# Performance work log

Measured on AMD Instinct MI355X. Metric: run time of the kernel, lower is better.

Reference implementation:

```python
import jax, jax.numpy as jnp
import numpy as np

N_Q = 8        # qubits
DENC = 3       # encoding entangling layers
DVAR = 3       # variational entangling layers
SEQ = 64
BATCH = 256
D_FEAT = N_Q * (DENC + 2)   # 40, per-token feature dim
D_W = N_Q * (DVAR + 2)      # 40, per-position weight dim


def _rx(t):
    c = jnp.cos(t / 2).astype(jnp.complex64)
    s = (-1j * jnp.sin(t / 2)).astype(jnp.complex64)
    return jnp.stack([jnp.stack([c, s]), jnp.stack([s, c])])


def _ry(t):
    c = jnp.cos(t / 2)
    s = jnp.sin(t / 2)
    return jnp.stack([jnp.stack([c, -s]), jnp.stack([s, c])]).astype(jnp.complex64)


def _apply1(state, U, wire):
    # state: (2,)*N_Q complex; apply 2x2 gate on `wire`
    s = jnp.tensordot(U, state, axes=([1], [wire]))
    return jnp.moveaxis(s, 0, wire)


def _cnot(state, c, t):
    s0 = jnp.take(state, 0, axis=c)
    s1 = jnpp_flip = jnp.take(state, 1, axis=c)
    t2 = t - 1 if t > c else t
    s1 = jnp.flip(s1, axis=t2)  # X on target when control=1
    return jnp.stack([s0, s1], axis=c)


def _circuit(x, w, sign):
    # x: [D_FEAT] encoding angles, w: [D_W] variational angles
    state = jnp.zeros((2,) * N_Q, jnp.complex64).at[(0,) * N_Q].set(1.0)
    idx = 0
    for j in range(N_Q):
        state = _apply1(state, _rx(x[idx]), j)
        state = _apply1(state, _ry(x[idx + 1]), j)
        idx += 2
    for _ in range(DENC):
        for j in range(N_Q):
            state = _cnot(state, j, (j + 1) % N_Q)
        for j in range(N_Q):
            state = _apply1(state, _ry(x[idx]), j)
            idx += 1
    idx = 0
    for j in range(N_Q):
        state = _apply1(state, _rx(w[idx]), j)
        state = _apply1(state, _ry(w[idx + 1]), j)
        idx += 2
    for _ in range(DVAR):
        for j in range(N_Q):
            state = _cnot(state, j, (j + 1) % N_Q)
        for j in range(N_Q):
            state = _apply1(state, _ry(w[idx]), j)
            idx += 1
    probs = (jnp.abs(state) ** 2).astype(jnp.float32)
    return jnp.sum(probs * sign)


# observable sign tables
_Z0 = jnp.array([1.0, -1.0], jnp.float32).reshape((2,) + (1,) * (N_Q - 1))
_ZALL = jnp.array([1.0, -1.0], jnp.float32)
for _ in range(N_Q - 1):
    _ZALL = _ZALL[..., None] * jnp.array([1.0, -1.0], jnp.float32)


def _batched(sign):
    f = lambda xx, ww: _circuit(xx, ww, sign)
    f = jax.vmap(f, in_axes=(0, 0))      # over seq positions (per-position weights)
    return jax.vmap(f, in_axes=(0, None))  # over batch


_qk = _batched(_Z0)
_v = _batched(_ZALL)  # random_op fixed deterministically to Z x Z x ... x Z


def setup_inputs() -> dict:
    key = jax.random.key(0)
    k1, k2, k3, k4 = jax.random.split(key, 4)
    scale = np.float32(np.pi / 4)
    x = jax.random.normal(k1, (BATCH, SEQ, D_FEAT), jnp.float32)
    pQ = scale * (2 * jax.random.normal(k2, (SEQ, D_W), jnp.float32) - 1)
    pK = scale * (2 * jax.random.normal(k3, (SEQ, D_W), jnp.float32) - 1)
    pV = scale * (2 * jax.random.normal(k4, (SEQ, D_W), jnp.float32) - 1)
    return {"x": x, "params_Q": pQ, "params_K": pK, "params_V": pV}


def reference(x, params_Q, params_K, params_V):
    # Per-token quantum circuit sims -> scalar Q, K, V expectations
    Q = _qk(x, params_Q)   # [B, S]
    K = _qk(x, params_K)   # [B, S]
    V = _v(x, params_V)    # [B, S]  (original returns d identical copies of this)
    # Gaussian-kernel attention: alpha[b,i,m] = exp(-(Q_i - K_m)^2)
    alpha = jnp.exp(-(Q[:, :, None] - K[:, None, :]) ** 2)   # [B, S, S]
    w = alpha / jnp.sum(alpha, axis=-1, keepdims=True)
    att = jnp.einsum('bim,bm->bi', w, V)                     # [B, S]
    return x + att[:, :, None]  # broadcast over d (V copies are identical)
```

## Files before the change

### kernel.cpp

```cpp
#include <hip/hip_runtime.h>

#define SEQd 64
#define BATCHd 256
#define DF 40

typedef float f2 __attribute__((ext_vector_type(2)));
typedef __fp16 h2v __attribute__((ext_vector_type(2)));


__device__ __forceinline__ f2 mkf2(float a, float b) { f2 r; r.x = a; r.y = b; return r; }

template<int LM>
__device__ __forceinline__ float xch1(float v) {
  if constexpr (LM == 0) {
    return v;
  } else if constexpr (LM == 1 || LM == 2 || LM == 3 || LM == 7 || LM == 15) {
    constexpr int ctrl = (LM == 1) ? 0xB1 : (LM == 2) ? 0x4E : (LM == 3) ? 0x1B
                       : (LM == 7) ? 0x141 : 0x140;
    return __int_as_float(__builtin_amdgcn_mov_dpp(__float_as_int(v), ctrl, 0xF, 0xF, true));
  } else if constexpr (LM == 4)  { return xch1<7>(xch1<3>(v));
  } else if constexpr (LM == 5)  { return xch1<7>(xch1<2>(v));
  } else if constexpr (LM == 6)  { return xch1<7>(xch1<1>(v));
  } else if constexpr (LM == 8)  { return xch1<15>(xch1<7>(v));
  } else if constexpr (LM == 12) { return xch1<15>(xch1<3>(v));
  } else if constexpr (LM == 13) { return xch1<15>(xch1<2>(v));
  } else if constexpr (LM == 14) { return xch1<15>(xch1<1>(v));
  } else {
    return __int_as_float(__builtin_amdgcn_ds_swizzle(__float_as_int(v), (LM << 10) | 0x1F));
  }
}

template<int LM>
__device__ __forceinline__ f2 xch2(f2 v) {
  if constexpr (LM == 0) return v;
  f2 r; r.x = xch1<LM>(v.x); r.y = xch1<LM>(v.y); return r;
}

__device__ __forceinline__ f2 pkmul(f2 a, f2 b) {
  f2 d;
  asm("v_pk_mul_f32 %0, %1, %2" : "=v"(d) : "v"(a), "v"(b));
  return d;
}
template<bool NEGB, bool SWAPA>
__device__ __forceinline__ f2 pkfma(f2 a, f2 b, f2 c) {
  f2 d;
  if constexpr (!NEGB && !SWAPA)
    asm("v_pk_fma_f32 %0, %1, %2, %3" : "=v"(d) : "v"(a), "v"(b), "v"(c));
  else if constexpr (NEGB && !SWAPA)
    asm("v_pk_fma_f32 %0, %1, %2, %3 neg_lo:[0,1,0] neg_hi:[0,1,0]"
        : "=v"(d) : "v"(a), "v"(b), "v"(c));
  else if constexpr (!NEGB && SWAPA)
    asm("v_pk_fma_f32 %0, %1, %2, %3 op_sel:[1,0,0] op_sel_hi:[0,1,1]"
        : "=v"(d) : "v"(a), "v"(b), "v"(c));
  else
    asm("v_pk_fma_f32 %0, %1, %2, %3 op_sel:[1,0,0] op_sel_hi:[0,1,1] neg_lo:[0,1,0] neg_hi:[0,1,0]"
        : "=v"(d) : "v"(a), "v"(b), "v"(c));
  return d;
}

__device__ __forceinline__ f2 cmul(f2 a, f2 b) {
  f2 r; r.x = a.x * b.x - a.y * b.y; r.y = a.x * b.y + a.y * b.x; return r;
}
__device__ __forceinline__ f2 uget(float4 f, bool bit) {
  f2 r; r.x = bit ? f.z : f.x; r.y = bit ? -f.w : f.y; return r;
}

template<int M, int SM, int J>
__device__ __forceinline__ void ry_rec(f2* rr, f2* ii, f2 CC, f2 TV) {
  if constexpr (J < 8) {
    constexpr int LM = M >> 4, RM = M & 15;
    constexpr int RJ = RM >> 1;
    constexpr bool R0 = (RM & 1) != 0;
    constexpr int JP = J ^ RJ;
    if constexpr (JP >= J) {
      constexpr int SRj = (SM & 15) >> 1;
      constexpr bool PJ = (__builtin_popcount(J & SRj) & 1) != 0;
      if constexpr (JP == J) {
        const f2 br = xch2<LM>(rr[J]);
        const f2 bi = xch2<LM>(ii[J]);
        rr[J] = pkfma<PJ, R0>(br, TV, pkmul(rr[J], CC));
        ii[J] = pkfma<PJ, R0>(bi, TV, pkmul(ii[J], CC));
      } else {
        constexpr bool PJP = (__builtin_popcount(JP & SRj) & 1) != 0;
        const f2 br0 = xch2<LM>(rr[JP]);
        const f2 bi0 = xch2<LM>(ii[JP]);
        const f2 br1 = xch2<LM>(rr[J]);
        const f2 bi1 = xch2<LM>(ii[J]);
        rr[J]  = pkfma<PJ,  R0>(br0, TV, pkmul(rr[J],  CC));
        ii[J]  = pkfma<PJ,  R0>(bi0, TV, pkmul(ii[J],  CC));
        rr[JP] = pkfma<PJP, R0>(br1, TV, pkmul(rr[JP], CC));
        ii[JP] = pkfma<PJP, R0>(bi1, TV, pkmul(ii[JP], CC));
      }
    }
    ry_rec<M, SM, J + 1>(rr, ii, CC, TV);
  }
}

template<int M, int SM>
__device__ __forceinline__ void ry16s(f2* rr, f2* ii, f2 cs, int lam) {
  constexpr int SL = SM >> 4;
  constexpr bool S0v = (SM & 1) != 0;
  float t0;
  if constexpr (SL != 0) t0 = (__popc(lam & SL) & 1) ? cs.y : -cs.y;
  else                   t0 = -cs.y;
  const f2 CC = mkf2(cs.x, cs.x);
  const f2 TV = mkf2(t0, S0v ? -t0 : t0);
  ry_rec<M, SM, 0>(rr, ii, CC, TV);
}

template<int M, int SM, int J>
__device__ __forceinline__ void su2_rec(f2* rr, f2* ii, f2 QX, f2 QW, f2 SC, f2 SB) {
  if constexpr (J < 8) {
    constexpr int LM = M >> 4, RM = M & 15;
    constexpr int RJ = RM >> 1;
    constexpr bool R0 = (RM & 1) != 0;
    constexpr int JP = J ^ RJ;
    if constexpr (JP >= J) {
      constexpr int SRj = (SM & 15) >> 1;
      constexpr bool PJ = (__builtin_popcount(J & SRj) & 1) != 0;
      if constexpr (JP == J) {
        const f2 br = xch2<LM>(rr[J]);
        const f2 bi = xch2<LM>(ii[J]);
        f2 t = pkmul(rr[J], QX);
        t = pkfma<!PJ, R0>(br, SC, t);
        t = pkfma<!PJ, false>(ii[J], SB, t);
        t = pkfma<false, R0>(bi, QW, t);
        f2 u = pkmul(ii[J], QX);
        u = pkfma<!PJ, R0>(bi, SC, u);
        u = pkfma<PJ, false>(rr[J], SB, u);
        u = pkfma<true, R0>(br, QW, u);
        rr[J] = t; ii[J] = u;
      } else {
        constexpr bool PJP = (__builtin_popcount(JP & SRj) & 1) != 0;
        const f2 br0 = xch2<LM>(rr[JP]);
        const f2 bi0 = xch2<LM>(ii[JP]);
        const f2 br1 = xch2<LM>(rr[J]);
        const f2 bi1 = xch2<LM>(ii[J]);
        f2 t0v = pkmul(rr[J], QX);
        t0v = pkfma<!PJ, R0>(br0, SC, t0v);
        t0v = pkfma<!PJ, false>(ii[J], SB, t0v);
        t0v = pkfma<false, R0>(bi0, QW, t0v);
        f2 u0v = pkmul(ii[J], QX);
        u0v = pkfma<!PJ, R0>(bi0, SC, u0v);
        u0v = pkfma<PJ, false>(rr[J], SB, u0v);
        u0v = pkfma<true, R0>(br0, QW, u0v);
        f2 t1v = pkmul(rr[JP], QX);
        t1v = pkfma<!PJP, R0>(br1, SC, t1v);
        t1v = pkfma<!PJP, false>(ii[JP], SB, t1v);
        t1v = pkfma<false, R0>(bi1, QW, t1v);
        f2 u1v = pkmul(ii[JP], QX);
        u1v = pkfma<!PJP, R0>(bi1, SC, u1v);
        u1v = pkfma<PJP, false>(rr[JP], SB, u1v);
        u1v = pkfma<true, R0>(br1, QW, u1v);
        rr[J] = t0v; ii[J] = u0v; rr[JP] = t1v; ii[JP] = u1v;
      }
    }
    su2_rec<M, SM, J + 1>(rr, ii, QX, QW, SC, SB);
  }
}

template<int M, int SM>
__device__ __forceinline__ void su2g(f2* rr, f2* ii, float4 q, int lam) {
  constexpr int SL = SM >> 4;
  constexpr bool S0v = (SM & 1) != 0;
  float sb, sc;
  if constexpr (SL != 0) {
    const bool p = (__popc(lam & SL) & 1) != 0;
    sb = p ? -q.y : q.y; sc = p ? -q.z : q.z;
  } else { sb = q.y; sc = q.z; }
  const f2 QX = mkf2(q.x, q.x), QW = mkf2(q.w, q.w);
  const f2 SCv = mkf2(sc, S0v ? -sc : sc);
  const f2 SBv = mkf2(sb, S0v ? -sb : sb);
  su2_rec<M, SM, 0>(rr, ii, QX, QW, SCv, SBv);
}

__device__ __forceinline__ void layers16s(f2* rr, f2* ii, const f2* L, int lam) {
  ry16s<0xC0,0x7F>(rr, ii, L[0],  lam);
  ry16s<0x60,0xC0>(rr, ii, L[1],  lam);
  ry16s<0x30,0xE0>(rr, ii, L[2],  lam);
  ry16s<0x18,0xF0>(rr, ii, L[3],  lam);
  ry16s<0x0C,0xF8>(rr, ii, L[4],  lam);
  ry16s<0x06,0xFC>(rr, ii, L[5],  lam);
  ry16s<0x03,0xFE>(rr, ii, L[6],  lam);
  ry16s<0xC1,0xFF>(rr, ii, L[7],  lam);
  ry16s<0xA0,0xD5>(rr, ii, L[8],  lam);
  ry16s<0x50,0xBF>(rr, ii, L[9],  lam);
  ry16s<0x28,0x5F>(rr, ii, L[10], lam);
  ry16s<0x14,0xAF>(rr, ii, L[11], lam);
  ry16s<0x0A,0x57>(rr, ii, L[12], lam);
  ry16s<0x05,0xAB>(rr, ii, L[13], lam);
  ry16s<0xC2,0x55>(rr, ii, L[14], lam);
  ry16s<0x61,0xAA>(rr, ii, L[15], lam);
  ry16s<0xF0,0x4C>(rr, ii, L[16], lam);
  ry16s<0x78,0x6A>(rr, ii, L[17], lam);
  ry16s<0x3C,0x35>(rr, ii, L[18], lam);
  ry16s<0x1E,0x9A>(rr, ii, L[19], lam);
  ry16s<0x0F,0xCD>(rr, ii, L[20], lam);
  ry16s<0xC7,0x66>(rr, ii, L[21], lam);
  ry16s<0xA3,0x33>(rr, ii, L[22], lam);
  ry16s<0x91,0x99>(rr, ii, L[23], lam);
}

__device__ __forceinline__ void initial16s(f2* rr, f2* ii, const float4* F, int lam) {
  su2g<0x80,0x80>(rr, ii, F[0], lam);
  su2g<0x40,0x40>(rr, ii, F[1], lam);
  su2g<0x20,0x20>(rr, ii, F[2], lam);
  su2g<0x10,0x10>(rr, ii, F[3], lam);
  su2g<0x08,0x08>(rr, ii, F[4], lam);
  su2g<0x04,0x04>(rr, ii, F[5], lam);
  su2g<0x02,0x02>(rr, ii, F[6], lam);
  su2g<0x01,0x01>(rr, ii, F[7], lam);
}

__device__ __forceinline__ void pinit16s(f2* rr, f2* ii, const float4* F, int lam) {
  f2 c = mkf2(1.f, 0.f);
#pragma unroll
  for (int i = 0; i < 4; ++i)
    c = cmul(c, uget(F[3 - i], ((lam >> i) & 1) != 0));
  f2 w67[4], w45[4];
#pragma unroll
  for (int j = 0; j < 4; ++j) {
    w67[j] = cmul(uget(F[6], (j & 2) != 0), uget(F[7], (j & 1) != 0));
    w45[j] = cmul(uget(F[4], (j & 2) != 0), uget(F[5], (j & 1) != 0));
  }
#pragma unroll
  for (int k = 0; k < 16; ++k) {
    const f2 u = w67[k & 3], w = w45[(k >> 2) & 3];
    f2 t = cmul(u, w);
    const f2 a = cmul(c, t);
    rr[k >> 1][k & 1] = a.x;
    ii[k >> 1][k & 1] = a.y;
  }
}

__device__ __forceinline__ uint32_t packh(float a, float b) {
  h2v h = __builtin_amdgcn_cvt_pkrtz(a, b);
  return __builtin_bit_cast(uint32_t, h);
}
__device__ __forceinline__ f2 unpackh(uint32_t u) {
  h2v h = __builtin_bit_cast(h2v, u);
  f2 r; r.x = (float)h[0]; r.y = (float)h[1]; return r;
}

__device__ __forceinline__ void snap_write16s(const f2* rr, const f2* ii,
                                              uint32_t* sn, int lam) {
  int tgt = 0;
  if (lam & 1) tgt ^= 0x33;
  if (lam & 2) tgt ^= 0x66;
  if (lam & 4) tgt ^= 0xCC;
  if (lam & 8) tgt ^= 0x19;
#pragma unroll
  for (int k = 0; k < 16; ++k) {
    const int rck = ((k & 1) ? 0x2B : 0) ^ ((k & 2) ? 0x56 : 0)
                  ^ ((k & 4) ? 0xAC : 0) ^ ((k & 8) ? 0xD9 : 0);
    sn[tgt ^ rck] = packh(rr[k >> 1][k & 1], ii[k >> 1][k & 1]);
  }
}

__device__ __forceinline__ void snap_read16s(f2* rr, f2* ii, const uint32_t* sn, int lam) {
  const uint4* p = (const uint4*)(sn + lam * 16);
#pragma unroll
  for (int t = 0; t < 4; ++t) {
    const uint4 w = p[t];
    const f2 a0 = unpackh(w.x), a1 = unpackh(w.y), a2 = unpackh(w.z), a3 = unpackh(w.w);
    rr[2 * t]     = mkf2(a0.x, a1.x);  ii[2 * t]     = mkf2(a0.y, a1.y);
    rr[2 * t + 1] = mkf2(a2.x, a3.x);  ii[2 * t + 1] = mkf2(a2.y, a3.y);
  }
}

template<int SM>
__device__ __forceinline__ float expect16s(const f2* rr, const f2* ii, int lam) {
  constexpr int SL = SM >> 4, SR4 = SM & 15;
  constexpr int SRj = SR4 >> 1;
  constexpr bool S0v = (SR4 & 1) != 0;
  float d = 0.f;
#pragma unroll
  for (int j = 0; j < 8; ++j) {
    const f2 pp = pkfma<false, false>(ii[j], ii[j], pkmul(rr[j], rr[j]));
    float contrib;
    if constexpr (S0v) contrib = pp.x - pp.y;
    else               contrib = pp.x + pp.y;
    const bool pj = (__builtin_popcount(j & SRj) & 1) != 0;
    d += pj ? -contrib : contrib;
  }
  float v;
  if constexpr (SL != 0) v = (__popc(lam & SL) & 1) ? -d : d;
  else                   v = d;
  v += xch1<1>(v); v += xch1<2>(v); v += xch1<4>(v); v += xch1<8>(v);
  return v;
}

__global__ __launch_bounds__(256) void prep_var(
    const float* __restrict__ pQ, const float* __restrict__ pK,
    const float* __restrict__ pV, float* __restrict__ vtab)
{
  const int t = blockIdx.x * 256 + threadIdx.x;
  if (t >= SEQd * 3 * 32) return;
  const int slot = t & 31;
  const int sh = t >> 5;
  const int h = sh % 3, sp = sh / 3;
  const float* w = ((h == 0) ? pQ : (h == 1) ? pK : pV) + sp * DF;
  float* o = vtab + sh * 80;
  if (slot < 8) {
    float cx, sx, cy, sy;
    __sincosf(w[2 * slot]     * 0.5f, &sx, &cx);
    __sincosf(w[2 * slot + 1] * 0.5f, &sy, &cy);
    ((float4*)o)[slot] = make_float4(cy * cx, sy * sx, sy * cx, cy * sx);
  } else {
    float sn, cn;
    __sincosf(w[16 + (slot - 8)] * 0.5f, &sn, &cn);
    ((float2*)(o + 32))[slot - 8] = make_float2(cn, sn);
  }
}

__global__ __launch_bounds__(256, 3) void qsal_mono(
    const float* __restrict__ x, const float* __restrict__ vtab,
    float* __restrict__ Qo, float* __restrict__ Ko, float* __restrict__ Vo)
{
  __shared__ __align__(16) float etab[16][84];
  __shared__ __align__(16) uint32_t snap[16][264];
  __shared__ __align__(16) float vtabs[240];
  const int tid = threadIdx.x;
  const int wid = tid >> 6, lane = tid & 63;
  const int lam = lane & 15;
  const int cig = (wid << 2) | (lane >> 4);
  const int s = blockIdx.x & 63;
  const int bbase = (blockIdx.x >> 6) << 4;

  for (int t = tid; t < 640; t += 256) {
    const int cc = t / 40, idx = t - cc * 40;
    const float ang = x[((size_t)(bbase + cc) * 64 + s) * 40 + idx];
    float sn, cn; __sincosf(ang * 0.5f, &sn, &cn);
    if (idx < 16) {
      const int wire = idx >> 1, isy = idx & 1;
      etab[cc][wire * 4 + isy * 2 + 0] = cn;
      etab[cc][wire * 4 + isy * 2 + 1] = sn;
    } else {
      etab[cc][32 + (idx - 16) * 2 + 0] = cn;
      etab[cc][32 + (idx - 16) * 2 + 1] = sn;
    }
  }
  if (tid < 60) ((float4*)vtabs)[tid] = ((const float4*)(vtab + s * 240))[tid];
  __syncthreads();
  if (tid < 128) {
    const int cc = tid >> 3, wire = tid & 7;
    float4* qt = (float4*)etab[cc];
    const float4 f = qt[wire];
    qt[wire] = make_float4(f.z * f.x, f.w * f.y, f.w * f.x, f.z * f.y);
  }
  __syncthreads();

  f2 rr[8], ii[8];
#pragma unroll 1
  for (int ph = 0; ph < 4; ++ph) {
    const f2* L;
    if (ph == 0) {
      pinit16s(rr, ii, (const float4*)etab[cig], lam);
      L = (const f2*)(etab[cig] + 32);
    } else {
      snap_read16s(rr, ii, snap[cig], lam);
      const float* th = vtabs + (ph - 1) * 80;
      initial16s(rr, ii, (const float4*)th, lam);
      L = (const f2*)(th + 32);
    }
    layers16s(rr, ii, L, lam);
    if (ph == 0) {
      snap_write16s(rr, ii, snap[cig], lam);
    } else {
      const float e = (ph == 3) ? expect16s<0x88>(rr, ii, lam)
                                : expect16s<0x4C>(rr, ii, lam);
      if (lam == 0) {
        float* op = (ph == 1) ? Qo : (ph == 2) ? Ko : Vo;
        op[(bbase + cig) * 64 + s] = e;
      }
    }
  }
}

__global__ __launch_bounds__(256) void qsal_attn(
    const float* __restrict__ x,
    const float* __restrict__ Qv,
    const float* __restrict__ Kv,
    const float* __restrict__ Vv,
    float* __restrict__ out)
{
  const int tid  = threadIdx.x;
  const int wid  = tid >> 6;
  const int lane = tid & 63;
  const int bi   = blockIdx.x * 4 + wid;
  const int b    = bi >> 6;

  const float q = Qv[bi];
  const float k = Kv[b * 64 + lane];
  const float v = Vv[b * 64 + lane];
  const float d = q - k;
  float e  = __expf(-d * d);
  float ev = e * v;
#pragma unroll
  for (int m = 1; m < 64; m <<= 1) {
    e  += __shfl_xor(e,  m, 64);
    ev += __shfl_xor(ev, m, 64);
  }
  const float att = ev / e;

  const size_t row = (size_t)bi * DF;
  if (lane < DF) out[row + lane] = x[row + lane] + att;
}

extern "C" void kernel_launch(void* const* d_in, const int* in_sizes, int n_in,
                              void* d_out, int out_size, void* d_ws, size_t ws_size,
                              hipStream_t stream) {
  const float* x  = (const float*)d_in[0];
  const float* pQ = (const float*)d_in[1];
  const float* pK = (const float*)d_in[2];
  const float* pV = (const float*)d_in[3];
  float* out = (float*)d_out;

  const int NC = BATCHd * SEQd;
  float* Qv   = (float*)d_ws;
  float* Kv   = Qv + NC;
  float* Vv   = Kv + NC;
  float* vtab = Vv + NC;

  prep_var<<<dim3(24), dim3(256), 0, stream>>>(pQ, pK, pV, vtab);
  qsal_mono<<<dim3(1024), dim3(256), 0, stream>>>(x, vtab, Qv, Kv, Vv);
  qsal_attn<<<dim3(NC / 4), dim3(256), 0, stream>>>(x, Qv, Kv, Vv, out);
}
```

Measured before the change: 82.94 us.

## Split monolithic circuit kernel into encoding and variational kernels via global snapshots

The single qsal_mono kernel is replaced, when the workspace is large enough, by two kernels. The first runs the encoding circuit per token and writes the packed state snapshot to global memory. The second launches three times as many blocks, each applying one of the Q/K/V variational circuits and computing its expectation. This aims to raise parallelism and occupancy (launch bounds 6) in the variational stage. In exchange it adds a 16 MB global round trip of snapshot data, plus an extra launch.

```diff
diff --git a/kernel.cpp b/kernel.cpp
--- a/kernel.cpp
+++ b/kernel.cpp
@@ -313,6 +313,83 @@
   }
 }
 
+__global__ __launch_bounds__(256, 3) void qsal_enc16(
+    const float* __restrict__ x, uint32_t* __restrict__ snapg)
+{
+  __shared__ __align__(16) float etab[16][84];
+  __shared__ __align__(16) uint32_t snap[16][264];
+  const int tid = threadIdx.x;
+  const int wid = tid >> 6, lane = tid & 63;
+  const int lam = lane & 15;
+  const int cig = (wid << 2) | (lane >> 4);
+  const int s = blockIdx.x & 63;
+  const int bbase = (blockIdx.x >> 6) << 4;
+
+  for (int t = tid; t < 640; t += 256) {
+    const int cc = t / 40, idx = t - cc * 40;
+    const float ang = x[((size_t)(bbase + cc) * 64 + s) * 40 + idx];
+    float sn, cn; __sincosf(ang * 0.5f, &sn, &cn);
+    if (idx < 16) {
+      const int wire = idx >> 1, isy = idx & 1;
+      etab[cc][wire * 4 + isy * 2 + 0] = cn;
+      etab[cc][wire * 4 + isy * 2 + 1] = sn;
+    } else {
+      etab[cc][32 + (idx - 16) * 2 + 0] = cn;
+      etab[cc][32 + (idx - 16) * 2 + 1] = sn;
+    }
+  }
+  __syncthreads();
+  if (tid < 128) {
+    const int cc = tid >> 3, wire = tid & 7;
+    float4* qt = (float4*)etab[cc];
+    const float4 f = qt[wire];
+    qt[wire] = make_float4(f.z * f.x, f.w * f.y, f.w * f.x, f.z * f.y);
+  }
+  __syncthreads();
+
+  f2 rr[8], ii[8];
+  pinit16s(rr, ii, (const float4*)etab[cig], lam);
+  layers16s(rr, ii, (const f2*)(etab[cig] + 32), lam);
+  snap_write16s(rr, ii, snap[cig], lam);
+
+  const int gw = (bbase + cig) * 64 + s;
+  uint4* gb = (uint4*)(snapg + (size_t)gw * 256);
+  const uint4* ls = (const uint4*)&snap[cig][lam * 16];
+#pragma unroll
+  for (int t = 0; t < 4; ++t) gb[lam * 4 + t] = ls[t];
+}
+
+__global__ __launch_bounds__(256, 6) void qsal_var16(
+    const uint32_t* __restrict__ snapg, const float* __restrict__ vtab,
+    float* __restrict__ Qo, float* __restrict__ Ko, float* __restrict__ Vo)
+{
+  __shared__ __align__(16) float ltab[84];
+  const int tid = threadIdx.x;
+  const int wid = tid >> 6, lane = tid & 63;
+  const int lam = lane & 15;
+  const int cig = (wid << 2) | (lane >> 4);
+  const int vb = blockIdx.x;
+  const int s = vb / 48;
+  const int j = vb - s * 48;
+  const int grp = j / 3, h = j - grp * 3;
+
+  if (tid < 20)
+    ((float4*)ltab)[tid] = ((const float4*)(vtab + (s * 3 + h) * 80))[tid];
+  __syncthreads();
+
+  const int gw = (grp * 16 + cig) * 64 + s;
+  f2 rr[8], ii[8];
+  snap_read16s(rr, ii, snapg + (size_t)gw * 256, lam);
+  initial16s(rr, ii, (const float4*)ltab, lam);
+  layers16s(rr, ii, (const f2*)(ltab + 32), lam);
+  const float e = (h == 2) ? expect16s<0x88>(rr, ii, lam)
+                           : expect16s<0x4C>(rr, ii, lam);
+  if (lam == 0) {
+    float* op = (h == 0) ? Qo : (h == 1) ? Ko : Vo;
+    op[gw] = e;
+  }
+}
+
 __global__ __launch_bounds__(256, 3) void qsal_mono(
     const float* __restrict__ x, const float* __restrict__ vtab,
     float* __restrict__ Qo, float* __restrict__ Ko, float* __restrict__ Vo)
@@ -421,8 +498,16 @@
   float* Kv   = Qv + NC;
   float* Vv   = Kv + NC;
   float* vtab = Vv + NC;
+  uint32_t* snapg = (uint32_t*)(vtab + SEQd * 3 * 80);
+
+  const size_t need = (size_t)(3 * NC + SEQd * 3 * 80) * 4 + (size_t)NC * 256 * 4;
 
   prep_var<<<dim3(24), dim3(256), 0, stream>>>(pQ, pK, pV, vtab);
-  qsal_mono<<<dim3(1024), dim3(256), 0, stream>>>(x, vtab, Qv, Kv, Vv);
+  if (ws_size >= need) {
+    qsal_enc16<<<dim3(1024), dim3(256), 0, stream>>>(x, snapg);
+    qsal_var16<<<dim3(3072), dim3(256), 0, stream>>>(snapg, vtab, Qv, Kv, Vv);
+  } else {
+    qsal_mono<<<dim3(1024), dim3(256), 0, stream>>>(x, vtab, Qv, Kv, Vv);
+  }
   qsal_attn<<<dim3(NC / 4), dim3(256), 0, stream>>>(x, Qv, Kv, Vv, out);
 }
```

Result: slower. 97.09 us (+17.1%).
